# Optimization experiments

Hardware: AMD Instinct MI355X
Metric: run time of the kernel (lower is better)

The kernel has to match this reference:

```python
import jax, jax.numpy as jnp
import numpy as np

D_MODEL = 768
N_HEADS = 12
HEAD = D_MODEL // N_HEADS  # 64


def setup_inputs() -> dict:
    key = jax.random.key(0)
    ks = jax.random.split(key, 9)
    s = 1.0 / np.sqrt(D_MODEL)
    x = jax.random.normal(ks[0], (2, 2048, D_MODEL), dtype=jnp.float32)
    # per-head Q/K/V projection weights stacked over heads: [H, d_model, head]
    Wq = jax.random.uniform(ks[1], (N_HEADS, D_MODEL, HEAD), minval=-s, maxval=s, dtype=jnp.float32)
    Wk = jax.random.uniform(ks[2], (N_HEADS, D_MODEL, HEAD), minval=-s, maxval=s, dtype=jnp.float32)
    Wv = jax.random.uniform(ks[3], (N_HEADS, D_MODEL, HEAD), minval=-s, maxval=s, dtype=jnp.float32)
    bq = jax.random.uniform(ks[4], (N_HEADS, HEAD), minval=-s, maxval=s, dtype=jnp.float32)
    bk = jax.random.uniform(ks[5], (N_HEADS, HEAD), minval=-s, maxval=s, dtype=jnp.float32)
    bv = jax.random.uniform(ks[6], (N_HEADS, HEAD), minval=-s, maxval=s, dtype=jnp.float32)
    Wo = jax.random.uniform(ks[7], (D_MODEL, D_MODEL), minval=-s, maxval=s, dtype=jnp.float32)
    bo = jax.random.uniform(ks[8], (D_MODEL,), minval=-s, maxval=s, dtype=jnp.float32)
    return {"x": x, "Wq": Wq, "Wk": Wk, "Wv": Wv, "bq": bq, "bk": bk, "bv": bv, "Wo": Wo, "bo": bo}


def reference(x, Wq, Wk, Wv, bq, bk, bv, Wo, bo):
    # x: [B, S, D]; weights stacked over heads [H, D, hd]
    Q = jnp.einsum('bsd,hde->bhse', x, Wq) + bq[None, :, None, :]
    K = jnp.einsum('bsd,hde->bhse', x, Wk) + bk[None, :, None, :]
    V = jnp.einsum('bsd,hde->bhse', x, Wv) + bv[None, :, None, :]
    scores = jnp.einsum('bhse,bhte->bhst', Q, K) / jnp.sqrt(jnp.float32(HEAD))
    attn = jax.nn.softmax(scores, axis=-1)  # [B, H, S, S]
    out = jnp.einsum('bhst,bhte->bhse', attn, V)  # [B, H, S, hd]
    B, H, S, E = out.shape
    out = out.transpose(0, 2, 1, 3).reshape(B, S, H * E)  # concat heads -> [B, S, D]
    return out @ Wo + bo
```

## Files before the change

kernel.cpp:

```cpp
#include <hip/hip_runtime.h>
#include <hip/hip_bf16.h>

typedef __bf16 bf16x8 __attribute__((ext_vector_type(8)));
typedef __bf16 bf16x4 __attribute__((ext_vector_type(4)));
typedef float  f32x4  __attribute__((ext_vector_type(4)));
typedef short  short4v __attribute__((ext_vector_type(4)));

#define MFMA_16x16x32(a,b,c) __builtin_amdgcn_mfma_f32_16x16x32_bf16((a),(b),(c),0,0,0)

#if __has_builtin(__builtin_amdgcn_mfma_f32_16x16x16_bf16)
__device__ inline f32x4 MFMA16(bf16x4 a, bf16x4 b, f32x4 c){
  return __builtin_amdgcn_mfma_f32_16x16x16_bf16(a, b, c, 0, 0, 0);
}
#elif __has_builtin(__builtin_amdgcn_mfma_f32_16x16x16bf16_1k)
__device__ inline f32x4 MFMA16(bf16x4 a, bf16x4 b, f32x4 c){
  return __builtin_amdgcn_mfma_f32_16x16x16bf16_1k(
      __builtin_bit_cast(short4v, a), __builtin_bit_cast(short4v, b), c, 0, 0, 0);
}
#else
__device__ inline f32x4 MFMA16(bf16x4 a, bf16x4 b, f32x4 c){
  f32x4 d;
  asm volatile("v_mfma_f32_16x16x16_bf16 %0, %1, %2, %3"
               : "=v"(d) : "v"(a), "v"(b), "v"(c));
  return d;
}
#endif

#if __has_builtin(__builtin_amdgcn_exp2f)
#define EXP2(x) __builtin_amdgcn_exp2f(x)
#else
extern "C" __device__ float __ocml_native_exp2_f32(float);
#define EXP2(x) __ocml_native_exp2_f32(x)
#endif

#if __has_builtin(__builtin_amdgcn_global_load_lds)
#define HAS_GLDS 1
__device__ inline void glds16(const __bf16* g, __bf16* l){
  __builtin_amdgcn_global_load_lds(
      (const __attribute__((address_space(1))) unsigned int*)g,
      (__attribute__((address_space(3))) unsigned int*)l, 16, 0, 0);
}
#else
#define HAS_GLDS 0
#endif

static constexpr int DM = 768;
static constexpr int NH = 12;
static constexpr int HD = 64;
static constexpr int BB = 2;
static constexpr int SS = 2048;
static constexpr int NR = BB*SS;
static constexpr int NC = 3*DM;
static constexpr int RTOT = BB*NH*SS;
static constexpr float SCALEQ = 0.125f * 1.4426950408889634f;

__device__ inline int xcd_swz(int b, int n){
  return (n % 8 == 0) ? (b % 8) * (n >> 3) + (b >> 3) : b;
}

static constexpr int PB_X = NR*DM/(4*256);
static constexpr int PB_W = 3*12*12;
static constexpr int PB_O = 12*12;
static constexpr int PB_B = (NC+255)/256;
__global__ __launch_bounds__(256) void k_prep(const float* __restrict__ x,
    const float* __restrict__ Wq, const float* __restrict__ Wk,
    const float* __restrict__ Wv, const float* __restrict__ bq,
    const float* __restrict__ bk, const float* __restrict__ bv,
    const float* __restrict__ Wo,
    __bf16* __restrict__ xb, __bf16* __restrict__ Wt,
    __bf16* __restrict__ WoT, float* __restrict__ bqkv)
{
  __shared__ float tile[64][65];
  const int blk = blockIdx.x, tid = threadIdx.x;
  if (blk < PB_X){
    int i = blk*256 + tid;
    float4 v = reinterpret_cast<const float4*>(x)[i];
    bf16x4 o; o[0]=(__bf16)v.x; o[1]=(__bf16)v.y; o[2]=(__bf16)v.z; o[3]=(__bf16)v.w;
    reinterpret_cast<bf16x4*>(xb)[i] = o;
  } else if (blk < PB_X + PB_W){
    int b2 = blk - PB_X;
    int dt = b2 % 12, h = (b2/12) % 12, m = b2/144;
    const float* W = (m==0)?Wq:((m==1)?Wk:Wv);
    float scale = (m==0)?SCALEQ:1.0f;
    int tx = tid & 63, ty = tid >> 6;
    #pragma unroll
    for (int i=0;i<16;i++){
      int dl = ty*16+i;
      tile[dl][tx] = W[(h*DM + dt*64 + dl)*HD + tx];
    }
    __syncthreads();
    #pragma unroll
    for (int i=0;i<16;i++){
      int e = ty*16+i;
      Wt[(size_t)(m*DM + h*HD + e)*DM + dt*64 + tx] = (__bf16)(tile[tx][e]*scale);
    }
  } else if (blk < PB_X + PB_W + PB_O){
    int b2 = blk - PB_X - PB_W;
    int dt = b2 % 12, ct = b2/12;
    int tx = tid & 63, ty = tid >> 6;
    #pragma unroll
    for (int i=0;i<16;i++){
      int dl = ty*16+i;
      tile[dl][tx] = Wo[(dt*64+dl)*DM + ct*64 + tx];
    }
    __syncthreads();
    #pragma unroll
    for (int i=0;i<16;i++){
      int cl = ty*16+i;
      WoT[(size_t)(ct*64+cl)*DM + dt*64 + tx] = (__bf16)tile[tx][cl];
    }
  } else {
    int c = (blk - PB_X - PB_W - PB_O)*256 + tid;
    if (c < NC){
      int m = c/DM, r = c - m*DM;
      const float* s = (m==0)?bq:((m==1)?bk:bv);
      bqkv[c] = s[r] * ((m==0)?SCALEQ:1.0f);
    }
  }
}

template<int BM, int EPI>
__global__ __launch_bounds__(256) void k_gemm(
    const __bf16* __restrict__ A, const __bf16* __restrict__ Bt,
    const float* __restrict__ bias, float* __restrict__ outF,
    __bf16* __restrict__ qb, __bf16* __restrict__ kb, __bf16* __restrict__ vb,
    int M, int N)
{
  constexpr int BN = 128, BK = 64;
  constexpr int K = DM;
  constexpr int HM = BM/2;
  constexpr int MR = BM/32;
  __shared__ __align__(16) __bf16 As[BM][BK];
  __shared__ __align__(16) __bf16 Bs[BN][BK];
  const int tid = threadIdx.x;
  const int w = tid>>6, lane = tid&63, g = lane>>4, r15 = lane&15;
  const int wr = w>>1, wc = w&1;
  const int nTM = M/BM;
  const int bx = xcd_swz(blockIdx.x, gridDim.x);
  const int mt = bx % nTM, nt = bx / nTM;
  const int m0 = mt*BM, n0 = nt*BN;

  const int rrel = lane>>3, seg = lane&7;
  const int ssrc = seg ^ rrel;

  f32x4 acc[MR][4];
  #pragma unroll
  for (int i=0;i<MR;i++)
    #pragma unroll
    for (int j=0;j<4;j++) acc[i][j] = f32x4{0.f,0.f,0.f,0.f};

  for (int k0=0;k0<K;k0+=BK){
#if HAS_GLDS
    #pragma unroll
    for (int c=0;c<BM/32;c++)
      glds16(&A[(size_t)(m0 + w*(BM/4) + c*8 + rrel)*K + k0 + ssrc*8],
             &As[w*(BM/4) + c*8][0]);
    #pragma unroll
    for (int c=0;c<4;c++)
      glds16(&Bt[(size_t)(n0 + w*32 + c*8 + rrel)*K + k0 + ssrc*8],
             &Bs[w*32 + c*8][0]);
#else
    #pragma unroll
    for (int c=0;c<BM/32;c++)
      *reinterpret_cast<uint4*>(&As[w*(BM/4) + c*8 + rrel][seg*8]) =
        *reinterpret_cast<const uint4*>(&A[(size_t)(m0 + w*(BM/4) + c*8 + rrel)*K + k0 + ssrc*8]);
    #pragma unroll
    for (int c=0;c<4;c++)
      *reinterpret_cast<uint4*>(&Bs[w*32 + c*8 + rrel][seg*8]) =
        *reinterpret_cast<const uint4*>(&Bt[(size_t)(n0 + w*32 + c*8 + rrel)*K + k0 + ssrc*8]);
#endif
    __syncthreads();
    bf16x8 af[MR][2], bfr[4][2];
    #pragma unroll
    for (int mi=0;mi<MR;mi++){
      int row = wr*HM + mi*16 + r15;
      #pragma unroll
      for (int c2=0;c2<2;c2++)
        af[mi][c2] = *reinterpret_cast<const bf16x8*>(&As[row][8*((c2*4+g) ^ (row&7))]);
    }
    #pragma unroll
    for (int ni=0;ni<4;ni++){
      int row = wc*64 + ni*16 + r15;
      #pragma unroll
      for (int c2=0;c2<2;c2++)
        bfr[ni][c2] = *reinterpret_cast<const bf16x8*>(&Bs[row][8*((c2*4+g) ^ (row&7))]);
    }
    #pragma unroll
    for (int c2=0;c2<2;c2++)
      #pragma unroll
      for (int mi=0;mi<MR;mi++)
        #pragma unroll
        for (int ni=0;ni<4;ni++)
          acc[mi][ni] = MFMA_16x16x32(af[mi][c2], bfr[ni][c2], acc[mi][ni]);
    __syncthreads();
  }

  #pragma unroll
  for (int mi=0;mi<MR;mi++){
    #pragma unroll
    for (int ni=0;ni<4;ni++){
      int row0 = m0 + wr*HM + mi*16 + 4*g;
      int col  = n0 + wc*64 + ni*16 + r15;
      float bc = bias[col];
      #pragma unroll
      for (int r=0;r<4;r++){
        float val = acc[mi][ni][r] + bc;
        int rr = row0 + r;
        if (EPI==1){
          outF[(size_t)rr*DM + col] = val;
        } else {
          int b = rr >> 11, s = rr & 2047;
          int m = col >= 2*DM ? 2 : (col >= DM ? 1 : 0);
          int c2 = col - m*DM, hh = c2>>6, ee = c2&63;
          __bf16* dst = (m==0) ? qb : ((m==1) ? kb : vb);
          dst[(((size_t)b*NH + hh)*SS + s)*HD + ee] = (__bf16)val;
        }
      }
    }
  }
}

__global__ __launch_bounds__(256) void k_vt(const __bf16* __restrict__ Vr,
                                            __bf16* __restrict__ Vt){
  __shared__ __align__(16) __bf16 tile[64][72];
  const int tid = threadIdx.x;
  const int bh = blockIdx.x >> 5, tt = blockIdx.x & 31;
  const int t0 = tt*64;
  const __bf16* src = Vr + (size_t)bh*SS*HD;
  __bf16* dst = Vt + (size_t)bh*HD*SS;
  const int rt = tid>>3, seg = tid&7;
  #pragma unroll
  for (int p=0;p<2;p++){
    int t = t0 + rt + 32*p;
    bf16x8 v = *reinterpret_cast<const bf16x8*>(&src[(size_t)t*HD + seg*8]);
    #pragma unroll
    for (int j=0;j<8;j++) tile[seg*8+j][rt+32*p] = v[j];
  }
  __syncthreads();
  #pragma unroll
  for (int p=0;p<2;p++){
    int e = rt + 32*p;
    *reinterpret_cast<uint4*>(&dst[(size_t)e*SS + t0 + seg*8]) =
      *reinterpret_cast<const uint4*>(&tile[e][seg*8]);
  }
}

__global__ __launch_bounds__(256) void k_attn(
    const __bf16* __restrict__ Qb, const __bf16* __restrict__ Kb,
    const __bf16* __restrict__ Vt, __bf16* __restrict__ AO, int kvLen)
{
  constexpr int TT = 64, SK = 72;
  __shared__ __align__(16) __bf16 Ks[2][TT][SK];
  __shared__ __align__(16) __bf16 Vs[2][HD][SK];
  const int tid = threadIdx.x, w = tid>>6, lane = tid&63, g = lane>>4, r15 = lane&15;
  const int bx = xcd_swz(blockIdx.x, gridDim.x);
  const int qt = bx & 15, bh = bx >> 4;
  const int q0 = qt*128 + w*32;
  const int kv0 = 0;
  const __bf16* Qh = Qb + (size_t)bh*SS*HD;
  const __bf16* Kh = Kb + (size_t)bh*SS*HD;
  const __bf16* Vh = Vt + (size_t)bh*HD*SS;

  bf16x8 qf[2][2];
  #pragma unroll
  for (int sub=0; sub<2; sub++){
    int qrow = q0 + sub*16 + r15;
    qf[sub][0] = *reinterpret_cast<const bf16x8*>(&Qh[qrow*HD + g*8]);
    qf[sub][1] = *reinterpret_cast<const bf16x8*>(&Qh[qrow*HD + 32 + g*8]);
  }

  f32x4 o[2][4];
  #pragma unroll
  for (int s2=0;s2<2;s2++)
    #pragma unroll
    for (int i=0;i<4;i++) o[s2][i] = f32x4{0.f,0.f,0.f,0.f};
  float psum[2] = {0.f, 0.f};

  const int row0 = tid>>3,        seg0 = tid&7;
  const int row1 = (tid+256)>>3,  seg1 = tid&7;
  const int vcol0 = 32*(seg0>>2) + 16*(seg0&1) + 4*((seg0>>1)&1);

  {
    uint4 k0v = *reinterpret_cast<const uint4*>(&Kh[(kv0+row0)*HD + seg0*8]);
    uint4 k1v = *reinterpret_cast<const uint4*>(&Kh[(kv0+row1)*HD + seg1*8]);
    uint4 v0v = *reinterpret_cast<const uint4*>(&Vh[(size_t)row0*SS + kv0 + seg0*8]);
    uint4 v1v = *reinterpret_cast<const uint4*>(&Vh[(size_t)row1*SS + kv0 + seg1*8]);
    *reinterpret_cast<uint4*>(&Ks[0][row0][seg0*8]) = k0v;
    *reinterpret_cast<uint4*>(&Ks[0][row1][seg1*8]) = k1v;
    *reinterpret_cast<uint2*>(&Vs[0][row0][vcol0])     = uint2{v0v.x, v0v.y};
    *reinterpret_cast<uint2*>(&Vs[0][row0][vcol0 + 8]) = uint2{v0v.z, v0v.w};
    *reinterpret_cast<uint2*>(&Vs[0][row1][vcol0])     = uint2{v1v.x, v1v.y};
    *reinterpret_cast<uint2*>(&Vs[0][row1][vcol0 + 8]) = uint2{v1v.z, v1v.w};
  }
  __syncthreads();

  int cur = 0;
  for (int t0 = kv0; t0 < kv0 + kvLen; t0 += TT){
    const bool hasNext = (t0 + TT) < kv0 + kvLen;
    uint4 k0v, k1v, v0v, v1v;
    if (hasNext){
      k0v = *reinterpret_cast<const uint4*>(&Kh[(t0+TT+row0)*HD + seg0*8]);
      k1v = *reinterpret_cast<const uint4*>(&Kh[(t0+TT+row1)*HD + seg1*8]);
      v0v = *reinterpret_cast<const uint4*>(&Vh[(size_t)row0*SS + t0+TT + seg0*8]);
      v1v = *reinterpret_cast<const uint4*>(&Vh[(size_t)row1*SS + t0+TT + seg1*8]);
    }

    bf16x8 kf0[4], kf1[4];
    #pragma unroll
    for (int jt=0;jt<4;jt++){
      kf0[jt] = *reinterpret_cast<const bf16x8*>(&Ks[cur][jt*16 + r15][g*8]);
      kf1[jt] = *reinterpret_cast<const bf16x8*>(&Ks[cur][jt*16 + r15][32 + g*8]);
    }
    bf16x8 vf[4][2];
    #pragma unroll
    for (int et=0;et<4;et++)
      #pragma unroll
      for (int p=0;p<2;p++)
        vf[et][p] = *reinterpret_cast<const bf16x8*>(&Vs[cur][et*16 + r15][p*32 + g*8]);

    f32x4 sc[2][4];
    __builtin_amdgcn_s_setprio(1);
    #pragma unroll
    for (int sub=0; sub<2; sub++)
      #pragma unroll
      for (int jt=0;jt<4;jt++){
        f32x4 t = f32x4{0.f,0.f,0.f,0.f};
        t = MFMA_16x16x32(kf0[jt], qf[sub][0], t);
        t = MFMA_16x16x32(kf1[jt], qf[sub][1], t);
        sc[sub][jt] = t;
      }
    __builtin_amdgcn_s_setprio(0);

    bf16x4 pa[2][4];
    #pragma unroll
    for (int sub=0; sub<2; sub++)
      #pragma unroll
      for (int ks=0;ks<4;ks++){
        float p0 = EXP2(sc[sub][ks][0]);
        float p1 = EXP2(sc[sub][ks][1]);
        float p2 = EXP2(sc[sub][ks][2]);
        float p3 = EXP2(sc[sub][ks][3]);
        pa[sub][ks][0] = (__bf16)p0; pa[sub][ks][1] = (__bf16)p1;
        pa[sub][ks][2] = (__bf16)p2; pa[sub][ks][3] = (__bf16)p3;
        psum[sub] += (p0 + p1) + (p2 + p3);
      }

    __builtin_amdgcn_s_setprio(1);
    #pragma unroll
    for (int sub=0; sub<2; sub++)
      #pragma unroll
      for (int et=0;et<4;et++)
        #pragma unroll
        for (int ks=0;ks<4;ks++){
          bf16x8 vv = vf[et][ks>>1];
          bf16x4 vq = (ks & 1) ? bf16x4{vv[4],vv[5],vv[6],vv[7]}
                               : bf16x4{vv[0],vv[1],vv[2],vv[3]};
          o[sub][et] = MFMA16(pa[sub][ks], vq, o[sub][et]);
        }
    __builtin_amdgcn_s_setprio(0);

    if (hasNext){
      int nxt = cur ^ 1;
      *reinterpret_cast<uint4*>(&Ks[nxt][row0][seg0*8]) = k0v;
      *reinterpret_cast<uint4*>(&Ks[nxt][row1][seg1*8]) = k1v;
      *reinterpret_cast<uint2*>(&Vs[nxt][row0][vcol0])     = uint2{v0v.x, v0v.y};
      *reinterpret_cast<uint2*>(&Vs[nxt][row0][vcol0 + 8]) = uint2{v0v.z, v0v.w};
      *reinterpret_cast<uint2*>(&Vs[nxt][row1][vcol0])     = uint2{v1v.x, v1v.y};
      *reinterpret_cast<uint2*>(&Vs[nxt][row1][vcol0 + 8]) = uint2{v1v.z, v1v.w};
    }
    __syncthreads();
    cur ^= 1;
  }

  const int b = bh/NH, h = bh - b*NH;
  #pragma unroll
  for (int sub=0; sub<2; sub++){
    float lv = psum[sub];
    lv += __shfl_xor(lv, 16);
    lv += __shfl_xor(lv, 32);
    float linv = 1.0f / lv;
    float li[4];
    #pragma unroll
    for (int r=0;r<4;r++) li[r] = __shfl(linv, 4*g + r);
    #pragma unroll
    for (int r=0;r<4;r++){
      int s = q0 + sub*16 + 4*g + r;
      #pragma unroll
      for (int et=0;et<4;et++)
        AO[((size_t)(b*SS + s))*DM + h*HD + et*16 + r15] = (__bf16)(o[sub][et][r]*li[r]);
    }
  }
}

extern "C" void kernel_launch(void* const* d_in, const int* in_sizes, int n_in,
                              void* d_out, int out_size, void* d_ws, size_t ws_size,
                              hipStream_t stream) {
  const float* x  = (const float*)d_in[0];
  const float* Wq = (const float*)d_in[1];
  const float* Wk = (const float*)d_in[2];
  const float* Wv = (const float*)d_in[3];
  const float* bq = (const float*)d_in[4];
  const float* bk = (const float*)d_in[5];
  const float* bv = (const float*)d_in[6];
  const float* Wo = (const float*)d_in[7];
  const float* bo = (const float*)d_in[8];
  float* out = (float*)d_out;

  char* ws = (char*)d_ws;
  size_t off = 0;
  auto alloc = [&](size_t bytes) -> void* {
    void* p = ws + off;
    off += (bytes + 255) & ~size_t(255);
    return p;
  };
  __bf16* xb   = (__bf16*)alloc((size_t)NR*DM*2);
  __bf16* wt   = (__bf16*)alloc((size_t)NC*DM*2);
  float*  bqkv = (float*) alloc((size_t)NC*4);
  __bf16* wot  = (__bf16*)alloc((size_t)DM*DM*2);
  __bf16* qb2  = (__bf16*)alloc((size_t)BB*NH*SS*HD*2);
  __bf16* kb2  = (__bf16*)alloc((size_t)BB*NH*SS*HD*2);
  __bf16* vb2  = (__bf16*)alloc((size_t)BB*NH*SS*HD*2);
  __bf16* vt2  = (__bf16*)alloc((size_t)BB*NH*SS*HD*2);
  __bf16* aob  = (__bf16*)alloc((size_t)NR*DM*2);

  k_prep<<<PB_X + PB_W + PB_O + PB_B, 256, 0, stream>>>(
      x, Wq, Wk, Wv, bq, bk, bv, Wo, xb, wt, wot, bqkv);

  k_gemm<128,0><<<(NR/128)*(NC/128), 256, 0, stream>>>(
      xb, wt, bqkv, nullptr, qb2, kb2, vb2, NR, NC);

  k_vt<<<BB*NH*(SS/64), 256, 0, stream>>>(vb2, vt2);

  k_attn<<<BB*NH*(SS/128), 256, 0, stream>>>(qb2, kb2, vt2, aob, SS);

  k_gemm<64,1><<<(NR/64)*(DM/128), 256, 0, stream>>>(
      aob, wot, bo, out, nullptr, nullptr, nullptr, NR, DM);
}
```

Measured before the change: 117.1 us.

## Fuse V transpose into QKV GEMM epilogue via shared-memory staging

```diff
diff --git a/kernel.cpp b/kernel.cpp
--- a/kernel.cpp
+++ b/kernel.cpp
@@ -51,7 +51,6 @@
 static constexpr int SS = 2048;
 static constexpr int NR = BB*SS;
 static constexpr int NC = 3*DM;
-static constexpr int RTOT = BB*NH*SS;
 static constexpr float SCALEQ = 0.125f * 1.4426950408889634f;
 
 __device__ inline int xcd_swz(int b, int n){
@@ -123,15 +122,18 @@
 __global__ __launch_bounds__(256) void k_gemm(
     const __bf16* __restrict__ A, const __bf16* __restrict__ Bt,
     const float* __restrict__ bias, float* __restrict__ outF,
-    __bf16* __restrict__ qb, __bf16* __restrict__ kb, __bf16* __restrict__ vb,
+    __bf16* __restrict__ qb, __bf16* __restrict__ kb, __bf16* __restrict__ vt,
     int M, int N)
 {
   constexpr int BN = 128, BK = 64;
   constexpr int K = DM;
   constexpr int HM = BM/2;
   constexpr int MR = BM/32;
-  __shared__ __align__(16) __bf16 As[BM][BK];
-  __shared__ __align__(16) __bf16 Bs[BN][BK];
+  union ShmU {
+    struct { __bf16 As[BM][BK]; __bf16 Bs[BN][BK]; } ab;
+    __bf16 Vl[(EPI==0)?128:1][136];
+  };
+  __shared__ ShmU u;
   const int tid = threadIdx.x;
   const int w = tid>>6, lane = tid&63, g = lane>>4, r15 = lane&15;
   const int wr = w>>1, wc = w&1;
@@ -154,19 +156,19 @@
     #pragma unroll
     for (int c=0;c<BM/32;c++)
       glds16(&A[(size_t)(m0 + w*(BM/4) + c*8 + rrel)*K + k0 + ssrc*8],
-             &As[w*(BM/4) + c*8][0]);
+             &u.ab.As[w*(BM/4) + c*8][0]);
     #pragma unroll
     for (int c=0;c<4;c++)
       glds16(&Bt[(size_t)(n0 + w*32 + c*8 + rrel)*K + k0 + ssrc*8],
-             &Bs[w*32 + c*8][0]);
+             &u.ab.Bs[w*32 + c*8][0]);
 #else
     #pragma unroll
     for (int c=0;c<BM/32;c++)
-      *reinterpret_cast<uint4*>(&As[w*(BM/4) + c*8 + rrel][seg*8]) =
+      *reinterpret_cast<uint4*>(&u.ab.As[w*(BM/4) + c*8 + rrel][seg*8]) =
         *reinterpret_cast<const uint4*>(&A[(size_t)(m0 + w*(BM/4) + c*8 + rrel)*K + k0 + ssrc*8]);
     #pragma unroll
     for (int c=0;c<4;c++)
-      *reinterpret_cast<uint4*>(&Bs[w*32 + c*8 + rrel][seg*8]) =
+      *reinterpret_cast<uint4*>(&u.ab.Bs[w*32 + c*8 + rrel][seg*8]) =
         *reinterpret_cast<const uint4*>(&Bt[(size_t)(n0 + w*32 + c*8 + rrel)*K + k0 + ssrc*8]);
 #endif
     __syncthreads();
@@ -176,14 +178,14 @@
       int row = wr*HM + mi*16 + r15;
       #pragma unroll
       for (int c2=0;c2<2;c2++)
-        af[mi][c2] = *reinterpret_cast<const bf16x8*>(&As[row][8*((c2*4+g) ^ (row&7))]);
+        af[mi][c2] = *reinterpret_cast<const bf16x8*>(&u.ab.As[row][8*((c2*4+g) ^ (row&7))]);
     }
     #pragma unroll
     for (int ni=0;ni<4;ni++){
       int row = wc*64 + ni*16 + r15;
       #pragma unroll
       for (int c2=0;c2<2;c2++)
-        bfr[ni][c2] = *reinterpret_cast<const bf16x8*>(&Bs[row][8*((c2*4+g) ^ (row&7))]);
+        bfr[ni][c2] = *reinterpret_cast<const bf16x8*>(&u.ab.Bs[row][8*((c2*4+g) ^ (row&7))]);
     }
     #pragma unroll
     for (int c2=0;c2<2;c2++)
@@ -193,6 +195,37 @@
         for (int ni=0;ni<4;ni++)
           acc[mi][ni] = MFMA_16x16x32(af[mi][c2], bfr[ni][c2], acc[mi][ni]);
     __syncthreads();
+  }
+
+  if constexpr (EPI==0){
+    if (nt >= 12){
+      #pragma unroll
+      for (int mi=0;mi<MR;mi++){
+        int rowl = wr*HM + mi*16 + 4*g;
+        #pragma unroll
+        for (int ni=0;ni<4;ni++){
+          int coll = wc*64 + ni*16 + r15;
+          float bc = bias[n0 + coll];
+          bf16x4 vv;
+          vv[0]=(__bf16)(acc[mi][ni][0]+bc); vv[1]=(__bf16)(acc[mi][ni][1]+bc);
+          vv[2]=(__bf16)(acc[mi][ni][2]+bc); vv[3]=(__bf16)(acc[mi][ni][3]+bc);
+          *reinterpret_cast<bf16x4*>(&u.Vl[coll][rowl]) = vv;
+        }
+      }
+      __syncthreads();
+      const int b = m0 >> 11, s0 = m0 & 2047;
+      const int c2base = (nt - 12) * 128;
+      #pragma unroll
+      for (int p=0;p<8;p++){
+        int chunk = p*256 + tid;
+        int rowl = chunk >> 4, segl = chunk & 15;
+        int c2 = c2base + rowl, hh = c2 >> 6, ee = c2 & 63;
+        *reinterpret_cast<uint4*>(
+            &vt[(((size_t)b*NH + hh)*HD + ee)*SS + s0 + segl*8]) =
+          *reinterpret_cast<const uint4*>(&u.Vl[rowl][segl*8]);
+      }
+      return;
+    }
   }
 
   #pragma unroll
@@ -210,38 +243,13 @@
           outF[(size_t)rr*DM + col] = val;
         } else {
           int b = rr >> 11, s = rr & 2047;
-          int m = col >= 2*DM ? 2 : (col >= DM ? 1 : 0);
+          int m = col >= DM ? 1 : 0;
           int c2 = col - m*DM, hh = c2>>6, ee = c2&63;
-          __bf16* dst = (m==0) ? qb : ((m==1) ? kb : vb);
+          __bf16* dst = (m==0) ? qb : kb;
           dst[(((size_t)b*NH + hh)*SS + s)*HD + ee] = (__bf16)val;
         }
       }
     }
-  }
-}
-
-__global__ __launch_bounds__(256) void k_vt(const __bf16* __restrict__ Vr,
-                                            __bf16* __restrict__ Vt){
-  __shared__ __align__(16) __bf16 tile[64][72];
-  const int tid = threadIdx.x;
-  const int bh = blockIdx.x >> 5, tt = blockIdx.x & 31;
-  const int t0 = tt*64;
-  const __bf16* src = Vr + (size_t)bh*SS*HD;
-  __bf16* dst = Vt + (size_t)bh*HD*SS;
-  const int rt = tid>>3, seg = tid&7;
-  #pragma unroll
-  for (int p=0;p<2;p++){
-    int t = t0 + rt + 32*p;
-    bf16x8 v = *reinterpret_cast<const bf16x8*>(&src[(size_t)t*HD + seg*8]);
-    #pragma unroll
-    for (int j=0;j<8;j++) tile[seg*8+j][rt+32*p] = v[j];
-  }
-  __syncthreads();
-  #pragma unroll
-  for (int p=0;p<2;p++){
-    int e = rt + 32*p;
-    *reinterpret_cast<uint4*>(&dst[(size_t)e*SS + t0 + seg*8]) =
-      *reinterpret_cast<const uint4*>(&tile[e][seg*8]);
   }
 }
 
@@ -419,7 +427,6 @@
   __bf16* wot  = (__bf16*)alloc((size_t)DM*DM*2);
   __bf16* qb2  = (__bf16*)alloc((size_t)BB*NH*SS*HD*2);
   __bf16* kb2  = (__bf16*)alloc((size_t)BB*NH*SS*HD*2);
-  __bf16* vb2  = (__bf16*)alloc((size_t)BB*NH*SS*HD*2);
   __bf16* vt2  = (__bf16*)alloc((size_t)BB*NH*SS*HD*2);
   __bf16* aob  = (__bf16*)alloc((size_t)NR*DM*2);
 
@@ -427,9 +434,7 @@
       x, Wq, Wk, Wv, bq, bk, bv, Wo, xb, wt, wot, bqkv);
 
   k_gemm<128,0><<<(NR/128)*(NC/128), 256, 0, stream>>>(
-      xb, wt, bqkv, nullptr, qb2, kb2, vb2, NR, NC);
-
-  k_vt<<<BB*NH*(SS/64), 256, 0, stream>>>(vb2, vt2);
+      xb, wt, bqkv, nullptr, qb2, kb2, vt2, NR, NC);
 
   k_attn<<<BB*NH*(SS/128), 256, 0, stream>>>(qb2, kb2, vt2, aob, SS);
 
```

Result: faster. 114.2 us, median of 2 (-2.5%).
